# Kernel tuning notes

Measured on AMD Instinct MI355X. Metric: run time of the kernel, lower is better.

## Reference

```python
import jax, jax.numpy as jnp
import numpy as np

EPSILON = 0.03   # entropic regularization
GAMMA = 0.5      # mass regularization
MAX_ITER = 10    # Sinkhorn iterations


def sinkhorn_unbalanced(feature1, feature2):
    # L2-normalize features
    f1 = feature1 / jnp.sqrt(jnp.sum(feature1 ** 2, -1, keepdims=True) + 1e-8)
    f2 = feature2 / jnp.sqrt(jnp.sum(feature2 ** 2, -1, keepdims=True) + 1e-8)
    C = 1.0 - jnp.einsum('bnc,bmc->bnm', f1, f2)       # cosine cost in [0, 2]
    K = jnp.exp(-C / EPSILON)                           # (B, N, M) Gibbs kernel
    B, N, M = K.shape
    power = GAMMA / (GAMMA + EPSILON)
    prob1 = jnp.full((B, N, 1), 1.0 / N, K.dtype)
    prob2 = jnp.full((B, M, 1), 1.0 / M, K.dtype)
    a = jnp.full((B, N, 1), 1.0 / N, K.dtype)
    b = jnp.full((B, M, 1), 1.0 / M, K.dtype)
    for _ in range(MAX_ITER):  # fixed small iteration count
        KTa = jnp.einsum('bnm,bno->bmo', K, a)
        b = (prob2 / (KTa + 1e-8)) ** power
        Kb = jnp.einsum('bnm,bmo->bno', K, b)
        a = (prob1 / (Kb + 1e-8)) ** power
    T = a * K * jnp.swapaxes(b, 1, 2)                   # transport plan (B, N, M)
    return T


def compute_rigid_transform(points1, points2, weights):
    # weighted SVD (Kabsch) on 3x3 covariances
    wn = weights[..., None] / (jnp.sum(weights[..., None], axis=1, keepdims=True) + 1e-5)
    centroid_a = jnp.sum(points1 * wn, axis=1)          # (B, 3)
    centroid_b = jnp.sum(points2 * wn, axis=1)
    a_c = points1 - centroid_a[:, None, :]
    b_c = points2 - centroid_b[:, None, :]
    cov = jnp.einsum('bnc,bnd->bcd', a_c, b_c * wn)     # (B, 3, 3)
    u, s, vh = jnp.linalg.svd(cov)
    v = jnp.swapaxes(vh, -1, -2)
    rot_pos = v @ jnp.swapaxes(u, -1, -2)
    v_neg = v.at[:, :, 2].multiply(-1.0)
    rot_neg = v_neg @ jnp.swapaxes(u, -1, -2)
    rot = jnp.where(jnp.linalg.det(rot_pos)[:, None, None] > 0, rot_pos, rot_neg)
    trans = -rot @ centroid_a[:, :, None] + centroid_b[:, :, None]
    return jnp.concatenate([rot, trans], axis=2)        # (B, 3, 4)


def setup_inputs() -> dict:
    key = jax.random.key(0)
    k1, k2, k3, k4 = jax.random.split(key, 4)
    B, N, M, C = 8, 4096, 4096, 256
    return {
        'feature1': jax.random.normal(k1, (B, N, C), jnp.float32),
        'feature2': jax.random.normal(k2, (B, M, C), jnp.float32),
        'points1': jax.random.normal(k3, (B, N, 3), jnp.float32),
        'points2': jax.random.normal(k4, (B, M, 3), jnp.float32),
    }


def reference(feature1, feature2, points1, points2):
    T = sinkhorn_unbalanced(feature1, feature2)          # (B, N, M)
    row_sum = jnp.sum(T, axis=-1, keepdims=True)         # (B, N, 1)
    corr = jnp.einsum('bnm,bmd->bnd', T, points2) / (row_sum + 1e-8)  # soft matches
    weights = jnp.squeeze(row_sum, -1)                   # (B, N)
    return compute_rigid_transform(points1, corr, weights)
```

## Files before the change

kernel.cpp:

```cpp
#include <hip/hip_runtime.h>

#define NB 8
#define NN 4096
#define MM 4096
#define CC 256
#define NPART 128

typedef unsigned short u16;
typedef __attribute__((ext_vector_type(4))) unsigned short u16x4;
typedef __attribute__((ext_vector_type(8))) short s16x8;
typedef __attribute__((ext_vector_type(4))) float f32x4;

#define INV_EPS 33.333333333333336f
#define EXP2_SCALE 48.089834696296504f
#define POWER   0.94339622641509435f
#define PROB    (1.0f/4096.0f)

static __device__ __forceinline__ float bf2f(u16 h) {
    union { unsigned int u; float f; } v;
    v.u = ((unsigned int)h) << 16;
    return v.f;
}
static __device__ __forceinline__ u16 f2bf(float f) {
    union { float f; unsigned int u; } v;
    v.f = f;
    unsigned int u = v.u;
    u += 0x7fffu + ((u >> 16) & 1u);
    return (u16)(u >> 16);
}
static __device__ __forceinline__ float gfun(float x) {
    return exp2f(POWER * log2f(PROB / (x + 1e-8f)));
}

__global__ __launch_bounds__(256) void norm_kernel(const float* __restrict__ src,
                                                   u16* __restrict__ dst)
{
    const int t = threadIdx.x, w = t >> 6, lane = t & 63;
    const size_t row = (size_t)blockIdx.x * 4 + w;
    const float* sp = src + row * CC + lane * 4;
    f32x4 v = *(const f32x4*)sp;
    float s = v.x * v.x + v.y * v.y + v.z * v.z + v.w * v.w;
    for (int o = 32; o > 0; o >>= 1) s += __shfl_xor(s, o);
    float rn = rsqrtf(s + 1e-8f);
    u16x4 o4;
    o4.x = f2bf(v.x * rn); o4.y = f2bf(v.y * rn);
    o4.z = f2bf(v.z * rn); o4.w = f2bf(v.w * rn);
    *(u16x4*)(dst + row * CC + lane * 4) = o4;
}

#define LDSS 68

__global__ __launch_bounds__(256, 2) void gemm_exp_kernel(
    const u16* __restrict__ f1s, const u16* __restrict__ f2s,
    u16* __restrict__ Ks, float* __restrict__ part)
{
    const int t = threadIdx.x;
    const int w = t >> 6, lane = t & 63;
    const int quad = lane >> 4, l15 = lane & 15;
    const int bx = blockIdx.x;
    const int by = blockIdx.y;
    const int ls = blockIdx.z;

    __shared__ u16 As[128 * LDSS];
    __shared__ u16 Bs[128 * LDSS];
    __shared__ float csum4[4][64];

    csum4[w][lane] = 0.f;

    const u16* f2base = f2s + ((size_t)ls * MM + (size_t)bx * 128) * CC;
    const u16* f1base = f1s + ((size_t)ls * NN + (size_t)by * 128) * CC;

    f32x4 acc[4][4];
#pragma unroll
    for (int i = 0; i < 4; ++i)
#pragma unroll
        for (int j = 0; j < 4; ++j) acc[i][j] = (f32x4){0.f, 0.f, 0.f, 0.f};

    const int g_r = t >> 3;
    const int g_c = (t & 7) << 3;

    for (int kt = 0; kt < 4; ++kt) {
        const int k0 = kt * 64;
        __syncthreads();
#pragma unroll
        for (int i = 0; i < 4; ++i) {
            const int row = g_r + i * 32;
            s16x8 va = *(const s16x8*)(f2base + (size_t)row * CC + k0 + g_c);
            s16x8 vb = *(const s16x8*)(f1base + (size_t)row * CC + k0 + g_c);
            *(s16x8*)&As[row * LDSS + g_c] = va;
            *(s16x8*)&Bs[row * LDSS + g_c] = vb;
        }
        __syncthreads();
#pragma unroll
        for (int s = 0; s < 2; ++s) {
            s16x8 af[4], bfr[4];
#pragma unroll
            for (int i = 0; i < 4; ++i)
                af[i] = *(const s16x8*)&As[((w & 1) * 64 + i * 16 + l15) * LDSS + s * 32 + quad * 8];
#pragma unroll
            for (int j = 0; j < 4; ++j)
                bfr[j] = *(const s16x8*)&Bs[((w >> 1) * 64 + j * 16 + l15) * LDSS + s * 32 + quad * 8];
#pragma unroll
            for (int i = 0; i < 4; ++i)
#pragma unroll
                for (int j = 0; j < 4; ++j)
                    acc[i][j] = __builtin_amdgcn_mfma_f32_16x16x32_bf16(af[i], bfr[j], acc[i][j], 0, 0, 0);
        }
    }

    u16* kb = Ks + (size_t)ls * NN * MM;
    const int rbase = by * 128 + (w >> 1) * 64 + l15;
    const int cbase = bx * 128 + (w & 1) * 64 + quad * 4;
    float partl[4][4];
#pragma unroll
    for (int i = 0; i < 4; ++i)
#pragma unroll
        for (int e = 0; e < 4; ++e) partl[i][e] = 0.f;

#pragma unroll
    for (int j = 0; j < 4; ++j) {
        const int r = rbase + j * 16;
#pragma unroll
        for (int i = 0; i < 4; ++i) {
            const int c = cbase + i * 16;
            f32x4 v = acc[i][j];
            const float e0 = exp2f((v.x - 1.f) * EXP2_SCALE);
            const float e1 = exp2f((v.y - 1.f) * EXP2_SCALE);
            const float e2 = exp2f((v.z - 1.f) * EXP2_SCALE);
            const float e3 = exp2f((v.w - 1.f) * EXP2_SCALE);
            u16x4 o;
            o.x = f2bf(e0); o.y = f2bf(e1); o.z = f2bf(e2); o.w = f2bf(e3);
            *(u16x4*)&kb[(size_t)r * MM + c] = o;
            partl[i][0] += e0; partl[i][1] += e1; partl[i][2] += e2; partl[i][3] += e3;
        }
    }

#pragma unroll
    for (int i = 0; i < 4; ++i)
#pragma unroll
        for (int e = 0; e < 4; ++e) {
            float v = partl[i][e];
            v += __shfl_xor(v, 1); v += __shfl_xor(v, 2);
            v += __shfl_xor(v, 4); v += __shfl_xor(v, 8);
            if (l15 == 0)
                csum4[w][i * 16 + quad * 4 + e] += v;
        }
    __syncthreads();
    if (t < 128) {
        const int half = t >> 6, local = t & 63;
        const float v = csum4[half][local] + csum4[half + 2][local];
        part[((size_t)ls * NPART + by) * MM + bx * 128 + t] = v * PROB;
    }
}

__global__ __launch_bounds__(256) void bfin_kernel(const float* __restrict__ part,
                                                   float* __restrict__ bvec,
                                                   int np4 )
{
    __shared__ float red[4][64];
    const int t = threadIdx.x;
    const int col = t & 63, pgrp = t >> 6;
    const int ls = blockIdx.x >> 6;
    const int cblk = blockIdx.x & 63;
    const int m = cblk * 64 + col;

    const float* pp = part + (size_t)ls * NPART * MM + (size_t)pgrp * np4 * MM + m;
    float s = 0.f;
#pragma unroll 8
    for (int p = 0; p < np4; ++p) s += pp[(size_t)p * MM];
    red[pgrp][col] = s;
    __syncthreads();
    if (t < 64) {
        const float S = red[0][t] + red[1][t] + red[2][t] + red[3][t];
        bvec[(size_t)ls * MM + cblk * 64 + t] = gfun(S);
    }
}

__global__ __launch_bounds__(256) void fused_kernel(const u16* __restrict__ Ks,
                                                    const float* __restrict__ bvec,
                                                    float* __restrict__ part)
{
    const int t = threadIdx.x, w = t >> 6, lane = t & 63;
    const int ls = blockIdx.x >> 7;
    const int chunk = blockIdx.x & 127;

    __shared__ float wp[2][4][4];

    const float* bp = bvec + (size_t)ls * MM + t * 16;
    float bv[16];
#pragma unroll
    for (int i = 0; i < 4; ++i) {
        f32x4 b4 = *(const f32x4*)(bp + i * 4);
        bv[i * 4 + 0] = b4.x; bv[i * 4 + 1] = b4.y;
        bv[i * 4 + 2] = b4.z; bv[i * 4 + 3] = b4.w;
    }
    float acc[16];
#pragma unroll
    for (int i = 0; i < 16; ++i) acc[i] = 0.f;

    const u16* kbase = Ks + ((size_t)ls * NN + (size_t)chunk * 32) * MM + t * 16;

    for (int rb = 0; rb < 8; ++rb) {
        const u16* kp = kbase + (size_t)(rb * 4) * MM;
        const int par = rb & 1;

        s16x8 kv[4][2];
#pragma unroll
        for (int r = 0; r < 4; ++r) {
            kv[r][0] = *(const s16x8*)(kp + (size_t)r * MM);
            kv[r][1] = *(const s16x8*)(kp + (size_t)r * MM + 8);
        }
#pragma unroll
        for (int r = 0; r < 4; ++r) {
            const u16* u0 = (const u16*)&kv[r][0];
            const u16* u1 = (const u16*)&kv[r][1];
            float s = 0.f;
#pragma unroll
            for (int i = 0; i < 8; ++i) s += bf2f(u0[i]) * bv[i];
#pragma unroll
            for (int i = 0; i < 8; ++i) s += bf2f(u1[i]) * bv[8 + i];
            for (int o = 32; o > 0; o >>= 1) s += __shfl_xor(s, o);
            if (lane == 0) wp[par][r][w] = s;
        }
        __syncthreads();

        float ar[4];
#pragma unroll
        for (int r = 0; r < 4; ++r) {
            const float S = wp[par][r][0] + wp[par][r][1]
                          + wp[par][r][2] + wp[par][r][3];
            ar[r] = gfun(S);
        }

#pragma unroll
        for (int r = 0; r < 4; ++r) {
            const u16* u0 = (const u16*)&kv[r][0];
            const u16* u1 = (const u16*)&kv[r][1];
#pragma unroll
            for (int i = 0; i < 8; ++i) acc[i]     += ar[r] * bf2f(u0[i]);
#pragma unroll
            for (int i = 0; i < 8; ++i) acc[8 + i] += ar[r] * bf2f(u1[i]);
        }
    }

    float* kout = part + ((size_t)ls * NPART + chunk) * MM + t * 16;
#pragma unroll
    for (int i = 0; i < 4; ++i)
        *(f32x4*)&kout[i * 4] =
            (f32x4){acc[i * 4 + 0], acc[i * 4 + 1], acc[i * 4 + 2], acc[i * 4 + 3]};
}

__global__ __launch_bounds__(256) void bp4_kernel(const float* __restrict__ bvec,
                                                  const float* __restrict__ p2,
                                                  float* __restrict__ bp4)
{
    const int t = blockIdx.x * 256 + threadIdx.x;
    const int ls = t >> 12;
    const int m = t & 4095;
    const float bv = bvec[t];
    const float x = p2[(size_t)t * 3 + 0];
    const float y = p2[(size_t)t * 3 + 1];
    const float z = p2[(size_t)t * 3 + 2];
    float* pb = bp4 + (size_t)ls * MM * 4;
    pb[m]          = bv;
    pb[MM + m]     = bv * x;
    pb[2 * MM + m] = bv * y;
    pb[3 * MM + m] = bv * z;
}

__global__ __launch_bounds__(256) void final_kernel(const u16* __restrict__ Ks,
                                                    const float* __restrict__ bp4,
                                                    float* __restrict__ wc4)
{
    __shared__ float planes[4][4096];
    const int t = threadIdx.x, w = t >> 6, lane = t & 63;
    const int ls = blockIdx.x >> 6;
    const int chunk = blockIdx.x & 63;

    const float* pb = bp4 + (size_t)ls * MM * 4;
#pragma unroll
    for (int p = 0; p < 4; ++p)
#pragma unroll
        for (int i = 0; i < 4; ++i) {
            const int idx = i * 1024 + t * 4;
            *(f32x4*)&planes[p][idx] = *(const f32x4*)(pb + p * MM + idx);
        }
    __syncthreads();

    for (int rr = 0; rr < 16; ++rr) {
        const int n = chunk * 64 + rr * 4 + w;
        const u16* kp = Ks + ((size_t)ls * NN + n) * MM;
        float s0 = 0.f, s1 = 0.f, s2 = 0.f, s3 = 0.f;
#pragma unroll 4
        for (int pass = 0; pass < 16; ++pass) {
            const int m = pass * 256 + lane * 4;
            u16x4 k4 = *(const u16x4*)(kp + m);
            f32x4 p0 = *(const f32x4*)&planes[0][m];
            f32x4 p1 = *(const f32x4*)&planes[1][m];
            f32x4 p2v = *(const f32x4*)&planes[2][m];
            f32x4 p3 = *(const f32x4*)&planes[3][m];
            const float k0 = bf2f(k4.x), k1 = bf2f(k4.y);
            const float k2 = bf2f(k4.z), k3 = bf2f(k4.w);
            s0 += k0 * p0.x + k1 * p0.y + k2 * p0.z + k3 * p0.w;
            s1 += k0 * p1.x + k1 * p1.y + k2 * p1.z + k3 * p1.w;
            s2 += k0 * p2v.x + k1 * p2v.y + k2 * p2v.z + k3 * p2v.w;
            s3 += k0 * p3.x + k1 * p3.y + k2 * p3.z + k3 * p3.w;
        }
        for (int o = 32; o > 0; o >>= 1) {
            s0 += __shfl_xor(s0, o); s1 += __shfl_xor(s1, o);
            s2 += __shfl_xor(s2, o); s3 += __shfl_xor(s3, o);
        }
        if (lane == 0) {
            const float av = gfun(s0);
            const float wgt = av * s0;
            const float inv = 1.f / (wgt + 1e-8f);
            f32x4 o = {av * s1 * inv, av * s2 * inv, av * s3 * inv, wgt};
            *(f32x4*)&wc4[((size_t)ls * NN + n) * 4] = o;
        }
    }
}

__global__ __launch_bounds__(256) void kabsch_kernel(const float* __restrict__ wc4,
                                                     const float* __restrict__ p1,
                                                     float* __restrict__ out)
{
    const int b = blockIdx.x;
    const int t = threadIdx.x, w = t >> 6, lane = t & 63;
    double acc[16];
#pragma unroll
    for (int k = 0; k < 16; ++k) acc[k] = 0.0;

    for (int n = t; n < NN; n += 256) {
        const float* wp = wc4 + ((size_t)b * NN + n) * 4;
        const float cx = wp[0], cy = wp[1], cz = wp[2], wgt = wp[3];
        const float* pp = p1 + ((size_t)b * NN + n) * 3;
        const double px = pp[0], py = pp[1], pz = pp[2];
        const double wd = wgt;
        const double wcx = wd * cx, wcy = wd * cy, wcz = wd * cz;
        acc[0] += wd;
        acc[1] += wd * px; acc[2] += wd * py; acc[3] += wd * pz;
        acc[4] += wcx;     acc[5] += wcy;     acc[6] += wcz;
        acc[7]  += px * wcx; acc[8]  += px * wcy; acc[9]  += px * wcz;
        acc[10] += py * wcx; acc[11] += py * wcy; acc[12] += py * wcz;
        acc[13] += pz * wcx; acc[14] += pz * wcy; acc[15] += pz * wcz;
    }

    __shared__ double red[4][16];
#pragma unroll
    for (int k = 0; k < 16; ++k) {
        double v = acc[k];
        for (int o = 32; o > 0; o >>= 1) v += __shfl_xor(v, o);
        acc[k] = v;
    }
    if (lane == 0)
        for (int k = 0; k < 16; ++k) red[w][k] = acc[k];
    __syncthreads();

    if (t == 0) {
        double S[16];
        for (int k = 0; k < 16; ++k)
            S[k] = red[0][k] + red[1][k] + red[2][k] + red[3][k];
        const double denom = S[0] + 1e-5;
        const double sfrac = S[0] / denom;
        double ca[3] = {S[1] / denom, S[2] / denom, S[3] / denom};
        double cb[3] = {S[4] / denom, S[5] / denom, S[6] / denom};
        double A[3][3], V[3][3];
        for (int i = 0; i < 3; ++i)
            for (int j = 0; j < 3; ++j) {
                A[i][j] = S[7 + i * 3 + j] / denom - (2.0 - sfrac) * ca[i] * cb[j];
                V[i][j] = (i == j) ? 1.0 : 0.0;
            }
        for (int sweep = 0; sweep < 20; ++sweep) {
            const int PP[3] = {0, 0, 1}, QQ[3] = {1, 2, 2};
            for (int r = 0; r < 3; ++r) {
                const int p = PP[r], q = QQ[r];
                double app = 0, aqq = 0, apq = 0;
                for (int i = 0; i < 3; ++i) {
                    app += A[i][p] * A[i][p];
                    aqq += A[i][q] * A[i][q];
                    apq += A[i][p] * A[i][q];
                }
                if (fabs(apq) < 1e-14 * (app + aqq) + 1e-300) continue;
                const double th = 0.5 * atan2(2.0 * apq, app - aqq);
                const double c = cos(th), sn = sin(th);
                for (int i = 0; i < 3; ++i) {
                    double x = A[i][p], y = A[i][q];
                    A[i][p] = c * x + sn * y; A[i][q] = -sn * x + c * y;
                    x = V[i][p]; y = V[i][q];
                    V[i][p] = c * x + sn * y; V[i][q] = -sn * x + c * y;
                }
            }
        }
        double sv[3];
        for (int j = 0; j < 3; ++j)
            sv[j] = sqrt(A[0][j] * A[0][j] + A[1][j] * A[1][j] + A[2][j] * A[2][j]);
        int idx[3] = {0, 1, 2};
        if (sv[idx[0]] < sv[idx[1]]) { int x = idx[0]; idx[0] = idx[1]; idx[1] = x; }
        if (sv[idx[0]] < sv[idx[2]]) { int x = idx[0]; idx[0] = idx[2]; idx[2] = x; }
        if (sv[idx[1]] < sv[idx[2]]) { int x = idx[1]; idx[1] = idx[2]; idx[2] = x; }
        double U[3][3], Vs[3][3];
        for (int j = 0; j < 3; ++j) {
            const int jj = idx[j];
            const double inv = 1.0 / fmax(sv[jj], 1e-300);
            for (int i = 0; i < 3; ++i) {
                U[i][j] = A[i][jj] * inv;
                Vs[i][j] = V[i][jj];
            }
        }
        double R[3][3];
        for (int i = 0; i < 3; ++i)
            for (int j = 0; j < 3; ++j)
                R[i][j] = Vs[i][0] * U[j][0] + Vs[i][1] * U[j][1] + Vs[i][2] * U[j][2];
        const double det = R[0][0] * (R[1][1] * R[2][2] - R[1][2] * R[2][1])
                         - R[0][1] * (R[1][0] * R[2][2] - R[1][2] * R[2][0])
                         + R[0][2] * (R[1][0] * R[2][1] - R[1][1] * R[2][0]);
        if (det < 0.0) {
            for (int i = 0; i < 3; ++i) Vs[i][2] = -Vs[i][2];
            for (int i = 0; i < 3; ++i)
                for (int j = 0; j < 3; ++j)
                    R[i][j] = Vs[i][0] * U[j][0] + Vs[i][1] * U[j][1] + Vs[i][2] * U[j][2];
        }
        double tr[3];
        for (int i = 0; i < 3; ++i)
            tr[i] = cb[i] - (R[i][0] * ca[0] + R[i][1] * ca[1] + R[i][2] * ca[2]);
        float* o = out + b * 12;
        for (int i = 0; i < 3; ++i) {
            o[i * 4 + 0] = (float)R[i][0];
            o[i * 4 + 1] = (float)R[i][1];
            o[i * 4 + 2] = (float)R[i][2];
            o[i * 4 + 3] = (float)tr[i];
        }
    }
}

extern "C" void kernel_launch(void* const* d_in, const int* in_sizes, int n_in,
                              void* d_out, int out_size, void* d_ws, size_t ws_size,
                              hipStream_t stream) {
    const float* f1 = (const float*)d_in[0];
    const float* f2 = (const float*)d_in[1];
    const float* p1 = (const float*)d_in[2];
    const float* p2 = (const float*)d_in[3];
    float* out = (float*)d_out;

    const size_t AL = 256;
    const size_t szK    = (size_t)NN * MM * 2;
    const size_t szF1   = (size_t)NN * CC * 2;
    const size_t szF2   = (size_t)MM * CC * 2;
    const size_t szB    = (size_t)MM * 4;
    const size_t szPart = (size_t)NPART * MM * 4;
    const size_t szBp4  = (size_t)MM * 16;
    const size_t szWc4  = (size_t)NN * 16;
    const size_t per_batch = szK + szF1 + szF2 + szB + szPart + szBp4 + szWc4 + 8 * AL;

    int NS = (int)(ws_size / per_batch);
    if (NS > NB) NS = NB;
    if (NS < 1) NS = 1;

    char* base = (char*)d_ws;
    size_t off = 0;
    auto carve = [&](size_t bytes) -> char* {
        char* p = base + off;
        off += (bytes + AL - 1) & ~(AL - 1);
        return p;
    };
    u16*   Ks   = (u16*)  carve((size_t)NS * szK);
    u16*   f1s  = (u16*)  carve((size_t)NS * szF1);
    u16*   f2s  = (u16*)  carve((size_t)NS * szF2);
    float* bvec = (float*)carve((size_t)NS * szB);
    float* part = (float*)carve((size_t)NS * szPart);
    float* bp4  = (float*)carve((size_t)NS * szBp4);
    float* wc4  = (float*)carve((size_t)NS * szWc4);

    for (int b0 = 0; b0 < NB; b0 += NS) {
        const int cnt = (NB - b0 < NS) ? (NB - b0) : NS;

        norm_kernel<<<cnt * NN / 4, 256, 0, stream>>>(f1 + (size_t)b0 * NN * CC, f1s);
        norm_kernel<<<cnt * MM / 4, 256, 0, stream>>>(f2 + (size_t)b0 * MM * CC, f2s);
        gemm_exp_kernel<<<dim3(MM / 128, NN / 128, cnt), 256, 0, stream>>>(f1s, f2s, Ks, part);
        bfin_kernel<<<cnt * 64, 256, 0, stream>>>(part, bvec, 8);

        for (int it = 0; it < 9; ++it) {
            fused_kernel<<<cnt * 128, 256, 0, stream>>>(Ks, bvec, part);
            bfin_kernel<<<cnt * 64, 256, 0, stream>>>(part, bvec, 32);
        }

        bp4_kernel<<<cnt * MM / 256, 256, 0, stream>>>(bvec, p2 + (size_t)b0 * MM * 3, bp4);
        final_kernel<<<cnt * 64, 256, 0, stream>>>(Ks, bp4, wc4);
        kabsch_kernel<<<cnt, 256, 0, stream>>>(wc4, p1 + (size_t)b0 * NN * 3, out + (size_t)b0 * 12);
    }

    (void)in_sizes; (void)n_in; (void)out_size;
}
```

Measured before the change: 972.4 us.

## Double-buffer K row loads and coalesce column layout in fused Sinkhorn kernel

In the fused Sinkhorn kernel, the loads of the next 4-row block of K are now issued before the current block is computed, using a two-slot register buffer. Each thread's 16 columns are split into two 8-wide halves 2048 columns apart, so adjacent lanes read adjacent 16-byte chunks and loads coalesce better. The GEMM+exp kernel's launch bound is also raised to 3 blocks per SM. The aim is to hide global memory latency, at the cost of more registers, which may lower occupancy or cause spills.

After: 2.037 ms. +109.5%, slower.

```diff
diff --git a/kernel.cpp b/kernel.cpp
--- a/kernel.cpp
+++ b/kernel.cpp
@@ -50,7 +50,7 @@
 
 #define LDSS 68
 
-__global__ __launch_bounds__(256, 2) void gemm_exp_kernel(
+__global__ __launch_bounds__(256, 3) void gemm_exp_kernel(
     const u16* __restrict__ f1s, const u16* __restrict__ f2s,
     u16* __restrict__ Ks, float* __restrict__ part)
 {
@@ -186,56 +186,69 @@
 
     __shared__ float wp[2][4][4];
 
-    const float* bp = bvec + (size_t)ls * MM + t * 16;
+    const float* bp = bvec + (size_t)ls * MM + t * 8;
     float bv[16];
 #pragma unroll
-    for (int i = 0; i < 4; ++i) {
-        f32x4 b4 = *(const f32x4*)(bp + i * 4);
-        bv[i * 4 + 0] = b4.x; bv[i * 4 + 1] = b4.y;
-        bv[i * 4 + 2] = b4.z; bv[i * 4 + 3] = b4.w;
+    for (int i = 0; i < 2; ++i) {
+        f32x4 b0 = *(const f32x4*)(bp + i * 2048);
+        f32x4 b1 = *(const f32x4*)(bp + i * 2048 + 4);
+        bv[i * 8 + 0] = b0.x; bv[i * 8 + 1] = b0.y;
+        bv[i * 8 + 2] = b0.z; bv[i * 8 + 3] = b0.w;
+        bv[i * 8 + 4] = b1.x; bv[i * 8 + 5] = b1.y;
+        bv[i * 8 + 6] = b1.z; bv[i * 8 + 7] = b1.w;
     }
     float acc[16];
 #pragma unroll
     for (int i = 0; i < 16; ++i) acc[i] = 0.f;
 
-    const u16* kbase = Ks + ((size_t)ls * NN + (size_t)chunk * 32) * MM + t * 16;
-
+    const u16* kbase = Ks + ((size_t)ls * NN + (size_t)chunk * 32) * MM + t * 8;
+
+    s16x8 kv[2][4][2];
+#pragma unroll
+    for (int r = 0; r < 4; ++r) {
+        kv[0][r][0] = *(const s16x8*)(kbase + (size_t)r * MM);
+        kv[0][r][1] = *(const s16x8*)(kbase + (size_t)r * MM + 2048);
+    }
+
+#pragma unroll
     for (int rb = 0; rb < 8; ++rb) {
-        const u16* kp = kbase + (size_t)(rb * 4) * MM;
-        const int par = rb & 1;
-
-        s16x8 kv[4][2];
+        const int cur = rb & 1, nxt = cur ^ 1;
+
+        if (rb < 7) {
+            const u16* kp = kbase + (size_t)((rb + 1) * 4) * MM;
+#pragma unroll
+            for (int r = 0; r < 4; ++r) {
+                kv[nxt][r][0] = *(const s16x8*)(kp + (size_t)r * MM);
+                kv[nxt][r][1] = *(const s16x8*)(kp + (size_t)r * MM + 2048);
+            }
+        }
+
 #pragma unroll
         for (int r = 0; r < 4; ++r) {
-            kv[r][0] = *(const s16x8*)(kp + (size_t)r * MM);
-            kv[r][1] = *(const s16x8*)(kp + (size_t)r * MM + 8);
-        }
-#pragma unroll
-        for (int r = 0; r < 4; ++r) {
-            const u16* u0 = (const u16*)&kv[r][0];
-            const u16* u1 = (const u16*)&kv[r][1];
+            const u16* u0 = (const u16*)&kv[cur][r][0];
+            const u16* u1 = (const u16*)&kv[cur][r][1];
             float s = 0.f;
 #pragma unroll
             for (int i = 0; i < 8; ++i) s += bf2f(u0[i]) * bv[i];
 #pragma unroll
             for (int i = 0; i < 8; ++i) s += bf2f(u1[i]) * bv[8 + i];
             for (int o = 32; o > 0; o >>= 1) s += __shfl_xor(s, o);
-            if (lane == 0) wp[par][r][w] = s;
+            if (lane == 0) wp[cur][r][w] = s;
         }
         __syncthreads();
 
         float ar[4];
 #pragma unroll
         for (int r = 0; r < 4; ++r) {
-            const float S = wp[par][r][0] + wp[par][r][1]
-                          + wp[par][r][2] + wp[par][r][3];
+            const float S = wp[cur][r][0] + wp[cur][r][1]
+                          + wp[cur][r][2] + wp[cur][r][3];
             ar[r] = gfun(S);
         }
 
 #pragma unroll
         for (int r = 0; r < 4; ++r) {
-            const u16* u0 = (const u16*)&kv[r][0];
-            const u16* u1 = (const u16*)&kv[r][1];
+            const u16* u0 = (const u16*)&kv[cur][r][0];
+            const u16* u1 = (const u16*)&kv[cur][r][1];
 #pragma unroll
             for (int i = 0; i < 8; ++i) acc[i]     += ar[r] * bf2f(u0[i]);
 #pragma unroll
@@ -243,11 +256,11 @@
         }
     }
 
-    float* kout = part + ((size_t)ls * NPART + chunk) * MM + t * 16;
-#pragma unroll
-    for (int i = 0; i < 4; ++i)
-        *(f32x4*)&kout[i * 4] =
-            (f32x4){acc[i * 4 + 0], acc[i * 4 + 1], acc[i * 4 + 2], acc[i * 4 + 3]};
+    float* kout = part + ((size_t)ls * NPART + chunk) * MM + t * 8;
+    *(f32x4*)&kout[0]    = (f32x4){acc[0],  acc[1],  acc[2],  acc[3]};
+    *(f32x4*)&kout[4]    = (f32x4){acc[4],  acc[5],  acc[6],  acc[7]};
+    *(f32x4*)&kout[2048] = (f32x4){acc[8],  acc[9],  acc[10], acc[11]};
+    *(f32x4*)&kout[2052] = (f32x4){acc[12], acc[13], acc[14], acc[15]};
 }
 
 __global__ __launch_bounds__(256) void bp4_kernel(const float* __restrict__ bvec,
```
